# Kernel tuning notes

Hardware: AMD Instinct MI355X
Metric: run time of the kernel (lower is better)

## Reference

```python
import jax, jax.numpy as jnp
import numpy as np

H = 512       # hidden_dim == node_init_dim
N_MAX = 128   # max nodes (upper bound on ADD_NODE count)
L = 1024      # action sequence length (padded with -1)
NEG = -1e9    # mask value for invalid destination logits


def _gru(x, h, wih, whh, bih, bhh):
    # PyTorch nn.GRUCell math; gates packed as [r, z, n] along dim 0.
    gi = wih @ x + bih
    gh = whh @ h + bhh
    d = h.shape[0]
    r = jax.nn.sigmoid(gi[:d] + gh[:d])
    z = jax.nn.sigmoid(gi[d:2 * d] + gh[d:2 * d])
    n = jnp.tanh(gi[2 * d:] + r * gh[2 * d:])
    return (1.0 - z) * n + z * h


def _make_actions(rng):
    # Synthesize a grammatically valid DGMG teacher-forcing trace:
    # ADD_NODE=0, ADD_EDGE=1, CHOOSE_DEST=2, STOP_EDGE=3, STOP_NODE=4, pad=-1
    acts, ags = [], []
    cur = -1
    while len(acts) < L - 8 and cur < N_MAX - 1:
        acts.append(0); ags.append(0)
        cur += 1
        if cur > 0:
            for _ in range(int(rng.integers(1, 4))):
                if len(acts) >= L - 4:
                    break
                acts.append(1); ags.append(0)
                acts.append(2); ags.append(int(rng.integers(0, cur)))
            acts.append(3); ags.append(0)
    acts.append(4); ags.append(0)
    pad = L - len(acts)
    acts += [-1] * pad
    ags += [0] * pad
    return np.array(acts, np.int64), np.array(ags, np.int64)


def setup_inputs() -> dict:
    rng = np.random.default_rng(0)
    acts, ags = _make_actions(rng)
    key = jax.random.key(0)
    ks = jax.random.split(key, 12)
    s = 0.02
    p = lambda k, shape: jax.random.normal(k, shape, jnp.float32) * s
    return {
        "actions": jnp.asarray(acts),
        "args_seq": jnp.asarray(ags),
        "node_init": p(ks[0], (H,)),
        "w_nip": p(ks[1], (H, H)), "b_nip": jnp.zeros((H,), jnp.float32),
        "w_e1": p(ks[2], (H, 2 * H)), "b_e1": jnp.zeros((H,), jnp.float32),
        "w_e2": p(ks[3], (2, H)), "b_e2": jnp.zeros((2,), jnp.float32),
        "w_q": p(ks[4], (H, 2 * H)), "b_q": jnp.zeros((H,), jnp.float32),
        "w_k": p(ks[5], (H, H)), "b_k": jnp.zeros((H,), jnp.float32),
        "wih_n": p(ks[6], (3 * H, H)), "whh_n": p(ks[7], (3 * H, H)),
        "bih_n": jnp.zeros((3 * H,), jnp.float32), "bhh_n": jnp.zeros((3 * H,), jnp.float32),
        "wih_g": p(ks[8], (3 * H, H)), "whh_g": p(ks[9], (3 * H, H)),
        "bih_g": jnp.zeros((3 * H,), jnp.float32), "bhh_g": jnp.zeros((3 * H,), jnp.float32),
        "graph0": jnp.zeros((H,), jnp.float32),
    }


def reference(actions, args_seq, node_init, w_nip, b_nip, w_e1, b_e1, w_e2, b_e2,
              w_q, b_q, w_k, b_k, wih_n, whh_n, bih_n, bhh_n,
              wih_g, whh_g, bih_g, bhh_g, graph0):
    h0 = w_nip @ node_init + b_nip  # same fresh-node embedding for every ADD_NODE
    idx_range = jnp.arange(N_MAX)

    def edge_logits(g, curv):
        h = jax.nn.relu(w_e1 @ jnp.concatenate([g, curv]) + b_e1)
        return w_e2 @ h + b_e2  # (2,)

    def add_node(carry, arg):
        g, ne, cur, nll = carry
        cur2 = cur + 1
        ne2 = ne.at[cur2].set(h0)
        g2 = _gru(h0, g, wih_g, whh_g, bih_g, bhh_g)
        return (g2, ne2, cur2, nll)

    def add_edge(carry, arg):
        g, ne, cur, nll = carry
        nll2 = nll - jax.nn.log_softmax(edge_logits(g, ne[cur]))[0]
        return (g, ne, cur, nll2)

    def choose_dest(carry, arg):
        g, ne, cur, nll = carry
        curv = ne[cur]
        q = w_q @ jnp.concatenate([g, curv]) + b_q           # (H,)
        k = ne @ w_k.T + b_k                                  # (N_MAX, H)
        logits = jnp.where(idx_range < cur, k @ q, NEG)       # mask nodes >= cur
        nll2 = nll - jax.nn.log_softmax(logits)[arg]
        chosen = ne[arg]
        new_cur = _gru(chosen, curv, wih_n, whh_n, bih_n, bhh_n)
        ne2 = ne.at[cur].set(new_cur)
        g2 = _gru(new_cur, g, wih_g, whh_g, bih_g, bhh_g)
        return (g2, ne2, cur, nll2)

    def stop_edge(carry, arg):
        g, ne, cur, nll = carry
        nll2 = nll - jax.nn.log_softmax(edge_logits(g, ne[cur]))[1]
        return (g, ne, cur, nll2)

    def noop(carry, arg):
        return carry

    branches = [add_node, add_edge, choose_dest, stop_edge, noop]

    def step(carry, inp):
        a, arg = inp
        idx = jnp.where((a < 0) | (a >= 4), 4, a).astype(jnp.int32)
        return jax.lax.switch(idx, branches, carry, arg), None

    init = (graph0, jnp.zeros((N_MAX, H), graph0.dtype),
            jnp.int32(-1), jnp.zeros((), graph0.dtype))
    (g, ne, cur, nll), _ = jax.lax.scan(
        step, init, (actions.astype(jnp.int32), args_seq.astype(jnp.int32)))
    return nll
```

## Files before the change

### kernel.cpp

```cpp
#include <hip/hip_runtime.h>
#include <math.h>

#define NBLK 64
#define NTHR 576
#define LSEQ 1024

typedef unsigned int u32;
typedef unsigned short u16;
typedef unsigned long long u64;

__device__ __forceinline__ float bf2f(u16 u){ union{u32 i;float f;}v; v.i=(u32)u<<16; return v.f; }
__device__ __forceinline__ u16 f2bf(float f){ union{float f;u32 i;}v; v.f=f; u32 x=v.i;
  return (u16)((x + 0x7fffu + ((x>>16)&1u)) >> 16); }
__device__ __forceinline__ float u2f(u32 u){ union{u32 i;float f;}v; v.i=u; return v.f; }
__device__ __forceinline__ u32  f2u(float f){ union{float f;u32 i;}v; v.f=f; return v.i; }
__device__ __forceinline__ float sigm(float x){ return 1.f/(1.f+__expf(-x)); }

__device__ __forceinline__ u64 gld64(const u64* p){ return __hip_atomic_load(const_cast<u64*>(p), __ATOMIC_RELAXED, __HIP_MEMORY_SCOPE_AGENT); }
__device__ __forceinline__ void gst64(u64* p, u64 v){ __hip_atomic_store(p, v, __ATOMIC_RELAXED, __HIP_MEMORY_SCOPE_AGENT); }
__device__ __forceinline__ u64 pollt(const u64* p, u32 tag){
  u64 v; int n = 0;
  do { v = gld64(p); } while ((u32)(v>>32) != tag && ++n < (1<<20));
  return v;
}

__device__ __forceinline__ float wred(float a){
  a += __int_as_float(__builtin_amdgcn_update_dpp(0, __float_as_int(a), 0x111, 0xf, 0xf, true));
  a += __int_as_float(__builtin_amdgcn_update_dpp(0, __float_as_int(a), 0x112, 0xf, 0xf, true));
  a += __int_as_float(__builtin_amdgcn_update_dpp(0, __float_as_int(a), 0x114, 0xf, 0xf, true));
  a += __int_as_float(__builtin_amdgcn_update_dpp(0, __float_as_int(a), 0x118, 0xf, 0xf, true));
  a += __int_as_float(__builtin_amdgcn_update_dpp(0, __float_as_int(a), 0x142, 0xa, 0xf, true));
  a += __int_as_float(__builtin_amdgcn_update_dpp(0, __float_as_int(a), 0x143, 0xc, 0xf, true));
  return __int_as_float(__builtin_amdgcn_readlane(__float_as_int(a), 63));
}
__device__ __forceinline__ float wredsh(float a){
  #pragma unroll
  for (int off = 32; off; off >>= 1) a += __shfl_xor(a, off);
  return a;
}
__device__ __forceinline__ float wredmaxsh(float a){
  #pragma unroll
  for (int off = 32; off; off >>= 1) a = fmaxf(a, __shfl_xor(a, off));
  return a;
}

__device__ __forceinline__ float dot8p(uint4 w, float4 a, float4 b2){
  float s;
  s  = u2f(w.x<<16)*a.x  + u2f(w.x&0xffff0000u)*a.y;
  s += u2f(w.y<<16)*a.z  + u2f(w.y&0xffff0000u)*a.w;
  s += u2f(w.z<<16)*b2.x + u2f(w.z&0xffff0000u)*b2.y;
  s += u2f(w.w<<16)*b2.z + u2f(w.w&0xffff0000u)*b2.w;
  return s;
}
__device__ __forceinline__ float dot4f(float4 w, float4 x){
  return w.x*x.x + w.y*x.y + w.z*x.z + w.w*x.w;
}
__device__ __forceinline__ uint4 pk8(float4 a, float4 b2){
  uint4 r;
  r.x = (u32)f2bf(a.x)  | ((u32)f2bf(a.y)<<16);
  r.y = (u32)f2bf(a.z)  | ((u32)f2bf(a.w)<<16);
  r.z = (u32)f2bf(b2.x) | ((u32)f2bf(b2.y)<<16);
  r.w = (u32)f2bf(b2.z) | ((u32)f2bf(b2.w)<<16);
  return r;
}

#define SMEM_BYTES 150048

#define RUN_JOBS() do { \
  if (wv == 8){ \
    if (dBV && b == dBo1){ \
      u64 v_ = pollt(XS + dBSlot*64 + lane, dBTag); \
      float x0 = sA0 + bf2f((u16)(v_ & 0xffff)); \
      float x1 = sA1 + bf2f((u16)((v_>>16) & 0xffff)); \
      x0 = (lane < dBcur) ? x0 : -__builtin_inff(); \
      x1 = (lane + 64 < dBcur) ? x1 : -__builtin_inff(); \
      float m_ = wredmaxsh(fmaxf(x0, x1)); \
      float s_ = wredsh(__expf(x0 - m_) + __expf(x1 - m_)); \
      float la_ = (dBarg < 64) ? __shfl(x0, dBarg) : __shfl(x1, dBarg - 64); \
      if (lane == 0) nllw += (m_ + logf(s_)) - la_; \
    } \
    if (dAV && (b == dAo1 || b == dAo2)){ \
      const u64* P_ = XP + ((size_t)(dASlot*64 + lane))*64 + ((b == dAo2) ? 32 : 0); \
      float h0_ = 0.f, h1_ = 0.f; \
      for (int c_ = 0; c_ < 2; ++c_){ \
        u64 vv_[16]; int bad_; int nn_ = 0; \
        do { bad_ = 0; \
          _Pragma("unroll") for (int j_ = 0; j_ < 16; ++j_) vv_[j_] = gld64(P_ + c_*16 + j_); \
          _Pragma("unroll") for (int j_ = 0; j_ < 16; ++j_) bad_ |= ((u32)(vv_[j_]>>32) != dATag); \
        } while (bad_ && ++nn_ < (1<<20)); \
        _Pragma("unroll") for (int j_ = 0; j_ < 16; ++j_){ \
          h0_ += bf2f((u16)(vv_[j_] & 0xffff)); h1_ += bf2f((u16)((vv_[j_]>>16) & 0xffff)); } \
      } \
      if (b == dAo2) gst64(XS + dASlot*64 + lane, ((u64)dATag<<32) | (u32)f2bf(h0_) | ((u32)f2bf(h1_)<<16)); \
      else { sA0 = h0_; sA1 = h1_; } \
    } \
    if (aeV && b == aeOwn){ \
      u64 v_ = pollt(XE + aeSlot*64 + lane, aeTag); \
      float p0_ = wredsh(bf2f((u16)(v_ & 0xffff))); \
      float p1_ = wredsh(bf2f((u16)((v_>>16) & 0xffff))); \
      if (lane == 0){ \
        float l0_ = p0_ + be2_0, l1_ = p1_ + be2_1; \
        float m_ = fmaxf(l0_, l1_); \
        nllw += m_ + logf(__expf(l0_-m_) + __expf(l1_-m_)) - (aeSel ? l1_ : l0_); \
      } \
    } \
  } \
} while(0)

#define SHIFT_JOBS() do { \
  dBV = dAV; dBSlot = dASlot; dBo1 = dAo1; dBTag = dATag; dBcur = dAcur; dBarg = dAarg; \
  dAV = 0; aeV = 0; \
} while(0)

__global__ void __launch_bounds__(NTHR, 1)
dgmg_kernel(const int* __restrict__ actions, const int* __restrict__ argseq,
            const float* __restrict__ node_init, const float* __restrict__ w_nip, const float* __restrict__ b_nip,
            const float* __restrict__ w_e1, const float* __restrict__ b_e1,
            const float* __restrict__ w_e2, const float* __restrict__ b_e2,
            const float* __restrict__ w_q, const float* __restrict__ b_q,
            const float* __restrict__ w_k,
            const float* __restrict__ wih_n, const float* __restrict__ whh_n,
            const float* __restrict__ bih_n, const float* __restrict__ bhh_n,
            const float* __restrict__ wih_g, const float* __restrict__ whh_g,
            const float* __restrict__ bih_g, const float* __restrict__ bhh_g,
            const float* __restrict__ graph0,
            float* __restrict__ out, unsigned char* __restrict__ ws)
{
  extern __shared__ unsigned char smem[];
  u16* s_wihg = (u16*)smem;
  u16* s_whhg = s_wihg + 24*512;
  u16* s_wihn = s_whhg + 24*512;
  u16* s_whhn = s_wihn + 24*512;
  u16* s_we1  = s_whhn + 24*512;
  u16* s_wq   = s_we1 + 8*1024;
  float* s_g    = (float*)(s_wq + 8*1024);
  float* s_nc   = s_g + 512;
  float* s_curv = s_nc + 512;
  float* s_h0   = s_curv + 512;
  float* s_kloc = s_h0 + 512;
  float* s_bihg = s_kloc + 1024;
  float* s_bhhg = s_bihg + 24;
  float* s_bihn = s_bhhg + 24;
  float* s_bhhn = s_bihn + 24;
  float* s_be1  = s_bhhn + 24;
  float* s_bq   = s_be1 + 8;
  float* s_q8   = s_bq + 8;
  float* s_red  = s_q8 + 8;
  u16*   s_gin  = (u16*)(s_red + 16);

  const int b = blockIdx.x, tid = threadIdx.x;
  const int wv = tid >> 6, lane = tid & 63;
  const int d = b*8 + ((wv < 8) ? wv : 0);

  u64* Xng = (u64*)ws;
  u64* Xh  = Xng + 2048;
  u64* XE  = Xh + 512;
  u64* XP  = XE + 256;
  u64* XS  = XP + 16384;
  u64* XN  = XS + 256;

  if (tid < 24){
    int ld = tid/3, gt = tid%3;
    int row = gt*512 + b*8 + ld;
    s_bihg[tid] = bih_g[row]; s_bhhg[tid] = bhh_g[row];
    s_bihn[tid] = bih_n[row]; s_bhhn[tid] = bhh_n[row];
  }
  if (tid < 8){ s_be1[tid] = b_e1[b*8+tid]; s_bq[tid] = b_q[b*8+tid]; }

  for (int r = wv; r < 24; r += 9){
    int ld = r/3, gt = r%3;
    long grow = (long)(gt*512 + b*8 + ld) * 512;
    float4 a0, a1;
    a0 = *(const float4*)&wih_g[grow + lane*8]; a1 = *(const float4*)&wih_g[grow + lane*8 + 4];
    *(uint4*)&s_wihg[r*512 + lane*8] = pk8(a0, a1);
    a0 = *(const float4*)&whh_g[grow + lane*8]; a1 = *(const float4*)&whh_g[grow + lane*8 + 4];
    *(uint4*)&s_whhg[r*512 + lane*8] = pk8(a0, a1);
    a0 = *(const float4*)&wih_n[grow + lane*8]; a1 = *(const float4*)&wih_n[grow + lane*8 + 4];
    *(uint4*)&s_wihn[r*512 + lane*8] = pk8(a0, a1);
    a0 = *(const float4*)&whh_n[grow + lane*8]; a1 = *(const float4*)&whh_n[grow + lane*8 + 4];
    *(uint4*)&s_whhn[r*512 + lane*8] = pk8(a0, a1);
  }
  if (wv < 8){
    long grow = (long)(b*8 + wv) * 1024;
    #pragma unroll
    for (int h = 0; h < 2; ++h){
      float4 a0 = *(const float4*)&w_e1[grow + h*512 + lane*8];
      float4 a1 = *(const float4*)&w_e1[grow + h*512 + lane*8 + 4];
      *(uint4*)&s_we1[wv*1024 + h*512 + lane*8] = pk8(a0, a1);
      float4 q0 = *(const float4*)&w_q[grow + h*512 + lane*8];
      float4 q1 = *(const float4*)&w_q[grow + h*512 + lane*8 + 4];
      *(uint4*)&s_wq[wv*1024 + h*512 + lane*8] = pk8(q0, q1);
    }
  }
  float we2_0 = w_e2[d], we2_1 = w_e2[512+d];
  float be2_0 = b_e2[0], be2_1 = b_e2[1];
  float nllw = 0.f, sA0 = 0.f, sA1 = 0.f;

  int aeV=0, aeSlot=0, aeSel=0, aeOwn=0; u32 aeTag=0;
  int dAV=0, dASlot=0, dAo1=0, dAo2=0, dAcur=0, dAarg=0; u32 dATag=0;
  int dBV=0, dBSlot=0, dBo1=0, dBcur=0, dBarg=0; u32 dBTag=0;
  int ecnt=0, dcnt=0;

  if (tid < 512) s_g[tid] = node_init[tid];
  __syncthreads();
  float cbg_r=0,cbg_z=0,bg_ni=0,bg_nh=0, bh_gr=0,bh_gz=0;
  float bn_r=0,bn_z=0,bn_nh=0, fb_r=0,fb_z=0,fb_n=0, be1w=0,bqw=0;
  if (wv < 8){
    cbg_r = s_bihg[wv*3+0]+s_bhhg[wv*3+0];
    cbg_z = s_bihg[wv*3+1]+s_bhhg[wv*3+1];
    bg_ni = s_bihg[wv*3+2]; bg_nh = s_bhhg[wv*3+2];
    bh_gr = s_bhhg[wv*3+0]; bh_gz = s_bhhg[wv*3+1];
    bn_r = s_bhhn[wv*3+0]; bn_z = s_bhhn[wv*3+1]; bn_nh = s_bhhn[wv*3+2];
    fb_r = s_bihn[wv*3+0]; fb_z = s_bihn[wv*3+1]; fb_n = s_bihn[wv*3+2];
    be1w = s_be1[wv]; bqw = s_bq[wv];
    const float* wr = w_nip + (long)d*512;
    float4 wa = *(const float4*)&wr[lane*8], wb2 = *(const float4*)&wr[lane*8+4];
    float4 xa = *(float4*)&s_g[lane*8], xb = *(float4*)&s_g[lane*8+4];
    float h0d = wred(dot4f(wa,xa)+dot4f(wb2,xb)) + b_nip[d];
    if (lane == 0) gst64(&Xh[d], (1ull<<32) | f2u(h0d));
  }
  u32 ph = 2;

  float gi0r=0,gi0z=0,gi0n=0, ghn0r=0,ghn0z=0,ghn0n=0;
  int cur = -1, have_se = 0;
  bool first_an = true;

  for (int t = 0; t < LSEQ; ++t){
    int a = actions[t];
    if (a == 1) continue;
    if (a == 3){ have_se = 1; continue; }
    if (a < 0 || a >= 4) continue;

    int t1 = (t+1 < LSEQ) ? actions[t+1] : -1;
    int nxt = (t1 == 1);
    int i2 = (t+2 < LSEQ) ? t+2 : LSEQ-1;
    int chn = nxt ? argseq[i2] : 0;

    if (a == 0){
      int eslot = ecnt & 3;
      u32 tg = ph-1; int par = tg & 1;
      if (first_an){
        if (tid < 512){ u64 v = pollt(&Xh[tid], 1u); s_h0[tid] = u2f((u32)v); s_g[tid] = graph0[tid]; }
      } else {
        if (tid < 512){ u64 v = pollt(&Xng[(par*512+tid)*2+1], tg); s_g[tid] = u2f((u32)v); }
      }
      __syncthreads();
      RUN_JOBS();
      if (wv < 8){
        float4 xg_a = *(float4*)&s_g[lane*8], xg_b = *(float4*)&s_g[lane*8+4];
        float4 xc_a = *(float4*)&s_curv[lane*8], xc_b = *(float4*)&s_curv[lane*8+4];
        const u32* Whg = (const u32*)s_whhg;
        if (first_an){
          float4 xh_a = *(float4*)&s_h0[lane*8], xh_b = *(float4*)&s_h0[lane*8+4];
          const u32* Wig = (const u32*)s_wihg; const u32* Wn = (const u32*)s_whhn;
          gi0r = wred(dot8p(*(const uint4*)&Wig[(wv*3+0)*256+lane*4], xh_a,xh_b)) + s_bihg[wv*3+0];
          gi0z = wred(dot8p(*(const uint4*)&Wig[(wv*3+1)*256+lane*4], xh_a,xh_b)) + s_bihg[wv*3+1];
          gi0n = wred(dot8p(*(const uint4*)&Wig[(wv*3+2)*256+lane*4], xh_a,xh_b)) + s_bihg[wv*3+2];
          ghn0r = wred(dot8p(*(const uint4*)&Wn[(wv*3+0)*256+lane*4], xh_a,xh_b)) + bn_r;
          ghn0z = wred(dot8p(*(const uint4*)&Wn[(wv*3+1)*256+lane*4], xh_a,xh_b)) + bn_z;
          ghn0n = wred(dot8p(*(const uint4*)&Wn[(wv*3+2)*256+lane*4], xh_a,xh_b)) + bn_nh;
        }
        {
          float ghr = wred(dot8p(*(const uint4*)&Whg[(wv*3+0)*256+lane*4], xg_a,xg_b)) + bh_gr;
          float ghz = wred(dot8p(*(const uint4*)&Whg[(wv*3+1)*256+lane*4], xg_a,xg_b)) + bh_gz;
          float ghn = wred(dot8p(*(const uint4*)&Whg[(wv*3+2)*256+lane*4], xg_a,xg_b)) + bg_nh;
          float r_ = sigm(gi0r + ghr), z_ = sigm(gi0z + ghz);
          float n_ = tanhf(gi0n + r_*ghn);
          if (lane == 0) gst64(&Xng[((ph&1)*512+d)*2+1], ((u64)ph<<32) | f2u((1.f-z_)*n_ + z_*s_g[d]));
        }
        if (nxt){
          float gr = bf2f(s_gin[chn*24+wv*3+0]), gz = bf2f(s_gin[chn*24+wv*3+1]), gn = bf2f(s_gin[chn*24+wv*3+2]);
          float r2 = sigm(gr + ghn0r), z2 = sigm(gz + ghn0z);
          float n2 = tanhf(gn + r2*ghn0n);
          if (lane == 0) gst64(&Xng[((ph&1)*512+d)*2], ((u64)ph<<32) | f2u((1.f-z2)*n2 + z2*s_h0[d]));
        }
        if (cur >= 0){
          const u32* Win = (const u32*)s_wihn;
          float fr = wred(dot8p(*(const uint4*)&Win[(wv*3+0)*256+lane*4], xc_a,xc_b)) + fb_r;
          float fz = wred(dot8p(*(const uint4*)&Win[(wv*3+1)*256+lane*4], xc_a,xc_b)) + fb_z;
          float fn = wred(dot8p(*(const uint4*)&Win[(wv*3+2)*256+lane*4], xc_a,xc_b)) + fb_n;
          const float* wkr = w_k + (long)d*512;
          float4 ka = *(const float4*)&wkr[lane*8], kb2 = *(const float4*)&wkr[lane*8+4];
          float kv = wred(dot4f(ka,xc_a)+dot4f(kb2,xc_b));
          if (lane == 0){
            s_gin[cur*24+wv*3+0] = f2bf(fr); s_gin[cur*24+wv*3+1] = f2bf(fz); s_gin[cur*24+wv*3+2] = f2bf(fn);
            s_kloc[wv*128 + cur] = kv;
          }
        }
        if (have_se){
          const u32* Re = (const u32*)s_we1 + wv*512;
          float pe = dot8p(*(const uint4*)&Re[lane*4], xg_a,xg_b) + dot8p(*(const uint4*)&Re[256+lane*4], xc_a,xc_b);
          float hv = fmaxf(wred(pe) + be1w, 0.f);
          if (lane == 0){ s_red[wv*2] = hv*we2_0; s_red[wv*2+1] = hv*we2_1; }
        }
      }
      __syncthreads();
      if (have_se && tid == 0){
        float p0 = 0.f, p1 = 0.f;
        #pragma unroll
        for (int i = 0; i < 8; ++i){ p0 += s_red[i*2]; p1 += s_red[i*2+1]; }
        gst64(&XE[eslot*64 + b], ((u64)ph<<32) | (u32)f2bf(p0) | ((u32)f2bf(p1)<<16));
      }
      if (tid < 512) s_curv[tid] = s_h0[tid];
      SHIFT_JOBS();
      if (have_se){ aeV=1; aeSlot=eslot; aeSel=1; aeOwn=ecnt&63; aeTag=ph; ecnt++; }
      have_se = 0; first_an = false;
      cur += 1; ph += 1;
    }
    else {
      int arg = argseq[t];
      int eslot = ecnt & 3, dslot = dcnt & 3;
      u32 tg = ph-1; int par = tg & 1;
      if (tid < 512){
        u64 v0, v1; int n = 0;
        const u64* p = &Xng[(par*512 + tid)*2];
        do { v0 = gld64(p); v1 = gld64(p+1); }
        while ((((u32)(v0>>32) != tg) || ((u32)(v1>>32) != tg)) && ++n < (1<<20));
        s_nc[tid] = u2f((u32)v0); s_g[tid] = u2f((u32)v1);
      }
      __syncthreads();
      RUN_JOBS();
      if (wv < 8){
        float4 xn_a = *(float4*)&s_nc[lane*8], xn_b = *(float4*)&s_nc[lane*8+4];
        float4 xg_a = *(float4*)&s_g[lane*8],  xg_b = *(float4*)&s_g[lane*8+4];
        float4 xc_a = *(float4*)&s_curv[lane*8], xc_b = *(float4*)&s_curv[lane*8+4];
        const u32* Wn = (const u32*)s_whhn; const u32* Wig = (const u32*)s_wihg; const u32* Whg = (const u32*)s_whhg;
        if (nxt){
          float ghr = wred(dot8p(*(const uint4*)&Wn[(wv*3+0)*256+lane*4], xn_a,xn_b)) + bn_r;
          float ghz = wred(dot8p(*(const uint4*)&Wn[(wv*3+1)*256+lane*4], xn_a,xn_b)) + bn_z;
          float ghn = wred(dot8p(*(const uint4*)&Wn[(wv*3+2)*256+lane*4], xn_a,xn_b)) + bn_nh;
          float gr = bf2f(s_gin[chn*24+wv*3+0]), gz = bf2f(s_gin[chn*24+wv*3+1]), gn = bf2f(s_gin[chn*24+wv*3+2]);
          float r_ = sigm(gr+ghr), z_ = sigm(gz+ghz);
          float n_ = tanhf(gn + r_*ghn);
          if (lane == 0) gst64(&Xng[((ph&1)*512+d)*2], ((u64)ph<<32) | f2u((1.f-z_)*n_ + z_*s_nc[d]));
        }
        {
          float pr = dot8p(*(const uint4*)&Wig[(wv*3+0)*256+lane*4], xn_a,xn_b)
                   + dot8p(*(const uint4*)&Whg[(wv*3+0)*256+lane*4], xg_a,xg_b);
          float pz = dot8p(*(const uint4*)&Wig[(wv*3+1)*256+lane*4], xn_a,xn_b)
                   + dot8p(*(const uint4*)&Whg[(wv*3+1)*256+lane*4], xg_a,xg_b);
          float r_ = sigm(wred(pr) + cbg_r);
          float z_ = sigm(wred(pz) + cbg_z);
          float gin_ = wred(dot8p(*(const uint4*)&Wig[(wv*3+2)*256+lane*4], xn_a,xn_b)) + bg_ni;
          float ghn_ = wred(dot8p(*(const uint4*)&Whg[(wv*3+2)*256+lane*4], xg_a,xg_b)) + bg_nh;
          float n_ = tanhf(gin_ + r_*ghn_);
          if (lane == 0) gst64(&Xng[((ph&1)*512+d)*2+1], ((u64)ph<<32) | f2u((1.f-z_)*n_ + z_*s_g[d]));
        }
        {
          const u32* Rq = (const u32*)s_wq + wv*512;
          float pq = dot8p(*(const uint4*)&Rq[lane*4], xg_a,xg_b) + dot8p(*(const uint4*)&Rq[256+lane*4], xc_a,xc_b);
          float qd = wred(pq) + bqw;
          const u32* Re = (const u32*)s_we1 + wv*512;
          float pe = dot8p(*(const uint4*)&Re[lane*4], xg_a,xg_b) + dot8p(*(const uint4*)&Re[256+lane*4], xc_a,xc_b);
          float hv = fmaxf(wred(pe) + be1w, 0.f);
          if (lane == 0){ s_q8[wv] = qd; s_red[wv*2] = hv*we2_0; s_red[wv*2+1] = hv*we2_1; }
        }
      }
      __syncthreads();
      if (tid < 64){
        float pl0 = 0.f, pl1 = 0.f;
        #pragma unroll
        for (int k = 0; k < 8; ++k){
          pl0 += s_kloc[k*128 + tid]      * s_q8[k];
          pl1 += s_kloc[k*128 + tid + 64] * s_q8[k];
        }
        gst64(&XP[((size_t)(dslot*64 + tid))*64 + b], ((u64)ph<<32) | (u32)f2bf(pl0) | ((u32)f2bf(pl1)<<16));
      }
      if (tid == 64){
        float p0 = 0.f, p1 = 0.f;
        #pragma unroll
        for (int i = 0; i < 8; ++i){ p0 += s_red[i*2]; p1 += s_red[i*2+1]; }
        gst64(&XE[eslot*64 + b], ((u64)ph<<32) | (u32)f2bf(p0) | ((u32)f2bf(p1)<<16));
      }
      if (tid < 512) s_curv[tid] = s_nc[tid];
      SHIFT_JOBS();
      aeV=1; aeSlot=eslot; aeSel=0; aeOwn=ecnt&63; aeTag=ph; ecnt++;
      dAV=1; dASlot=dslot; dAo1=(2*dcnt)&63; dAo2=(2*dcnt+1)&63; dAcur=cur; dAarg=arg; dATag=ph;
      dcnt++;
      ph += 1;
    }
  }

  {
    int eslot = ecnt & 3;
    u32 tg = ph-1; int par = tg & 1;
    if (tid < 512){ u64 v = pollt(&Xng[(par*512+tid)*2+1], tg); s_g[tid] = u2f((u32)v); }
    __syncthreads();
    RUN_JOBS();
    if (have_se && wv < 8){
      float4 xg_a = *(float4*)&s_g[lane*8], xg_b = *(float4*)&s_g[lane*8+4];
      float4 xc_a = *(float4*)&s_curv[lane*8], xc_b = *(float4*)&s_curv[lane*8+4];
      const u32* Re = (const u32*)s_we1 + wv*512;
      float pe = dot8p(*(const uint4*)&Re[lane*4], xg_a,xg_b) + dot8p(*(const uint4*)&Re[256+lane*4], xc_a,xc_b);
      float hv = fmaxf(wred(pe) + be1w, 0.f);
      if (lane == 0){ s_red[wv*2] = hv*we2_0; s_red[wv*2+1] = hv*we2_1; }
    }
    __syncthreads();
    if (have_se && tid == 0){
      float p0 = 0.f, p1 = 0.f;
      #pragma unroll
      for (int i = 0; i < 8; ++i){ p0 += s_red[i*2]; p1 += s_red[i*2+1]; }
      gst64(&XE[eslot*64 + b], ((u64)ph<<32) | (u32)f2bf(p0) | ((u32)f2bf(p1)<<16));
    }
    SHIFT_JOBS();
    RUN_JOBS();
    if (wv == 8){
      if (have_se && b == 0){
        u64 v = pollt(&XE[eslot*64 + lane], ph);
        float p0 = wredsh(bf2f((u16)(v & 0xffff)));
        float p1 = wredsh(bf2f((u16)((v>>16) & 0xffff)));
        if (lane == 0){
          float l0 = p0 + be2_0, l1 = p1 + be2_1;
          float m = fmaxf(l0, l1);
          nllw += m + logf(__expf(l0-m) + __expf(l1-m)) - l1;
        }
      }
      if (lane == 0) gst64(&XN[b], (0xFFFFull<<32) | f2u(nllw));
      if (b == 0){
        u64 v = pollt(&XN[lane], 0xFFFFu);
        float tot = wredsh(u2f((u32)v));
        if (lane == 0) out[0] = tot;
      }
    }
  }
}

extern "C" void kernel_launch(void* const* d_in, const int* in_sizes, int n_in,
                              void* d_out, int out_size, void* d_ws, size_t ws_size,
                              hipStream_t stream) {
  (void)in_sizes; (void)n_in; (void)out_size; (void)ws_size;
  hipMemsetAsync(d_ws, 0, 156160, stream);
  hipFuncSetAttribute((const void*)dgmg_kernel,
                      hipFuncAttributeMaxDynamicSharedMemorySize, SMEM_BYTES);
  dgmg_kernel<<<NBLK, NTHR, SMEM_BYTES, stream>>>(
      (const int*)d_in[0], (const int*)d_in[1],
      (const float*)d_in[2], (const float*)d_in[3], (const float*)d_in[4],
      (const float*)d_in[5], (const float*)d_in[6],
      (const float*)d_in[7], (const float*)d_in[8],
      (const float*)d_in[9], (const float*)d_in[10],
      (const float*)d_in[11],
      (const float*)d_in[13], (const float*)d_in[14],
      (const float*)d_in[15], (const float*)d_in[16],
      (const float*)d_in[17], (const float*)d_in[18],
      (const float*)d_in[19], (const float*)d_in[20],
      (const float*)d_in[21],
      (float*)d_out, (unsigned char*)d_ws);
}
```

Before: 1.102 ms.

## Split auxiliary softmax/NLL jobs across extra waves with deeper pipeline

Raises the block to 11 waves and gives the edge-logit NLL, the partial-sum reduction and the dest softmax their own waves (8, 9, 10), so they no longer run back to back on one wave. The dest reduction becomes a three-stage pipeline through two XS halves, and leftover jobs are drained after the loop. It also reorders the per-step GRU work so the critical graph GRU output is published first, and reuses the freshly computed input projection when the next chosen node is the current one. The cost is more threads per block, an extra block-wide sync after init, a larger workspace, and longer latency before final NLL terms are summed.

```diff
diff --git a/kernel.cpp b/kernel.cpp
--- a/kernel.cpp
+++ b/kernel.cpp
@@ -2,7 +2,7 @@
 #include <math.h>
 
 #define NBLK 64
-#define NTHR 576
+#define NTHR 704
 #define LSEQ 1024
 
 typedef unsigned int u32;
@@ -67,49 +67,52 @@
 #define SMEM_BYTES 150048
 
 #define RUN_JOBS() do { \
-  if (wv == 8){ \
-    if (dBV && b == dBo1){ \
-      u64 v_ = pollt(XS + dBSlot*64 + lane, dBTag); \
-      float x0 = sA0 + bf2f((u16)(v_ & 0xffff)); \
-      float x1 = sA1 + bf2f((u16)((v_>>16) & 0xffff)); \
-      x0 = (lane < dBcur) ? x0 : -__builtin_inff(); \
-      x1 = (lane + 64 < dBcur) ? x1 : -__builtin_inff(); \
-      float m_ = wredmaxsh(fmaxf(x0, x1)); \
-      float s_ = wredsh(__expf(x0 - m_) + __expf(x1 - m_)); \
-      float la_ = (dBarg < 64) ? __shfl(x0, dBarg) : __shfl(x1, dBarg - 64); \
-      if (lane == 0) nllw += (m_ + logf(s_)) - la_; \
-    } \
-    if (dAV && (b == dAo1 || b == dAo2)){ \
-      const u64* P_ = XP + ((size_t)(dASlot*64 + lane))*64 + ((b == dAo2) ? 32 : 0); \
-      float h0_ = 0.f, h1_ = 0.f; \
-      for (int c_ = 0; c_ < 2; ++c_){ \
-        u64 vv_[16]; int bad_; int nn_ = 0; \
-        do { bad_ = 0; \
-          _Pragma("unroll") for (int j_ = 0; j_ < 16; ++j_) vv_[j_] = gld64(P_ + c_*16 + j_); \
-          _Pragma("unroll") for (int j_ = 0; j_ < 16; ++j_) bad_ |= ((u32)(vv_[j_]>>32) != dATag); \
-        } while (bad_ && ++nn_ < (1<<20)); \
-        _Pragma("unroll") for (int j_ = 0; j_ < 16; ++j_){ \
-          h0_ += bf2f((u16)(vv_[j_] & 0xffff)); h1_ += bf2f((u16)((vv_[j_]>>16) & 0xffff)); } \
-      } \
-      if (b == dAo2) gst64(XS + dASlot*64 + lane, ((u64)dATag<<32) | (u32)f2bf(h0_) | ((u32)f2bf(h1_)<<16)); \
-      else { sA0 = h0_; sA1 = h1_; } \
-    } \
-    if (aeV && b == aeOwn){ \
-      u64 v_ = pollt(XE + aeSlot*64 + lane, aeTag); \
-      float p0_ = wredsh(bf2f((u16)(v_ & 0xffff))); \
-      float p1_ = wredsh(bf2f((u16)((v_>>16) & 0xffff))); \
-      if (lane == 0){ \
-        float l0_ = p0_ + be2_0, l1_ = p1_ + be2_1; \
-        float m_ = fmaxf(l0_, l1_); \
-        nllw += m_ + logf(__expf(l0_-m_) + __expf(l1_-m_)) - (aeSel ? l1_ : l0_); \
-      } \
+  if (wv == 8 && d2V && (b == d2o1 || b == d2o2)){ \
+    int half_ = (b == d2o2) ? 1 : 0; \
+    const u64* P_ = XP + ((size_t)(d2Slot*64 + lane))*64 + half_*32; \
+    u64 vv_[32]; int bad_; int nn_ = 0; \
+    do { bad_ = 0; \
+      _Pragma("unroll") for (int j_ = 0; j_ < 32; ++j_) vv_[j_] = gld64(P_ + j_); \
+      _Pragma("unroll") for (int j_ = 0; j_ < 32; ++j_) bad_ |= ((u32)(vv_[j_]>>32) != d2Tag); \
+    } while (bad_ && ++nn_ < (1<<20)); \
+    float h0_ = 0.f, h1_ = 0.f; \
+    _Pragma("unroll") for (int j_ = 0; j_ < 32; ++j_){ \
+      h0_ += bf2f((u16)(vv_[j_] & 0xffff)); h1_ += bf2f((u16)((vv_[j_]>>16) & 0xffff)); } \
+    gst64(&XS[half_*256 + d2Slot*64 + lane], ((u64)d2Tag<<32) | (u32)f2bf(h0_) | ((u32)f2bf(h1_)<<16)); \
+  } \
+  if (wv == 10 && d3V && b == d3o1){ \
+    const u64* pa_ = &XS[d3Slot*64 + lane]; \
+    const u64* pb_ = &XS[256 + d3Slot*64 + lane]; \
+    u64 va_, vb_; int nn_ = 0; \
+    do { va_ = gld64(pa_); vb_ = gld64(pb_); } \
+    while ((((u32)(va_>>32) != d3Tag) || ((u32)(vb_>>32) != d3Tag)) && ++nn_ < (1<<20)); \
+    float x0 = bf2f((u16)(va_ & 0xffff)) + bf2f((u16)(vb_ & 0xffff)); \
+    float x1 = bf2f((u16)((va_>>16) & 0xffff)) + bf2f((u16)((vb_>>16) & 0xffff)); \
+    x0 = (lane < d3cur)      ? x0 : -__builtin_inff(); \
+    x1 = (lane + 64 < d3cur) ? x1 : -__builtin_inff(); \
+    float m_ = wredmaxsh(fmaxf(x0, x1)); \
+    float s_ = wredsh(__expf(x0 - m_) + __expf(x1 - m_)); \
+    float la_ = (d3arg < 64) ? __shfl(x0, d3arg) : __shfl(x1, d3arg - 64); \
+    if (lane == 0) nllw += (m_ + logf(s_)) - la_; \
+  } \
+  if (wv == 9 && e2V && b == e2Own){ \
+    u64 v_ = pollt(XE + e2Slot*64 + lane, e2Tag); \
+    float p0_ = wredsh(bf2f((u16)(v_ & 0xffff))); \
+    float p1_ = wredsh(bf2f((u16)((v_>>16) & 0xffff))); \
+    if (lane == 0){ \
+      float l0_ = p0_ + be2_0, l1_ = p1_ + be2_1; \
+      float m_ = fmaxf(l0_, l1_); \
+      nllw += m_ + logf(__expf(l0_-m_) + __expf(l1_-m_)) - (e2Sel ? l1_ : l0_); \
     } \
   } \
 } while(0)
 
-#define SHIFT_JOBS() do { \
-  dBV = dAV; dBSlot = dASlot; dBo1 = dAo1; dBTag = dATag; dBcur = dAcur; dBarg = dAarg; \
-  dAV = 0; aeV = 0; \
+#define SHIFT3() do { \
+  d3V=d2V; d3Slot=d2Slot; d3o1=d2o1; d3Tag=d2Tag; d3cur=d2cur; d3arg=d2arg; \
+  d2V=d1V; d2Slot=d1Slot; d2o1=d1o1; d2o2=d1o2; d2Tag=d1Tag; d2cur=d1cur; d2arg=d1arg; \
+  d1V=0; \
+  e2V=e1V; e2Slot=e1Slot; e2Own=e1Own; e2Tag=e1Tag; e2Sel=e1Sel; \
+  e1V=0; \
 } while(0)
 
 __global__ void __launch_bounds__(NTHR, 1)
@@ -157,7 +160,7 @@
   u64* XE  = Xh + 512;
   u64* XP  = XE + 256;
   u64* XS  = XP + 16384;
-  u64* XN  = XS + 256;
+  u64* XN  = XS + 512;
 
   if (tid < 24){
     int ld = tid/3, gt = tid%3;
@@ -167,7 +170,7 @@
   }
   if (tid < 8){ s_be1[tid] = b_e1[b*8+tid]; s_bq[tid] = b_q[b*8+tid]; }
 
-  for (int r = wv; r < 24; r += 9){
+  for (int r = wv; r < 24; r += 11){
     int ld = r/3, gt = r%3;
     long grow = (long)(gt*512 + b*8 + ld) * 512;
     float4 a0, a1;
@@ -194,11 +197,13 @@
   }
   float we2_0 = w_e2[d], we2_1 = w_e2[512+d];
   float be2_0 = b_e2[0], be2_1 = b_e2[1];
-  float nllw = 0.f, sA0 = 0.f, sA1 = 0.f;
-
-  int aeV=0, aeSlot=0, aeSel=0, aeOwn=0; u32 aeTag=0;
-  int dAV=0, dASlot=0, dAo1=0, dAo2=0, dAcur=0, dAarg=0; u32 dATag=0;
-  int dBV=0, dBSlot=0, dBo1=0, dBcur=0, dBarg=0; u32 dBTag=0;
+  float nllw = 0.f;
+
+  int d1V=0,d1Slot=0,d1o1=0,d1o2=0,d1cur=0,d1arg=0; u32 d1Tag=0;
+  int d2V=0,d2Slot=0,d2o1=0,d2o2=0,d2cur=0,d2arg=0; u32 d2Tag=0;
+  int d3V=0,d3Slot=0,d3o1=0,d3cur=0,d3arg=0; u32 d3Tag=0;
+  int e1V=0,e1Slot=0,e1Own=0,e1Sel=0; u32 e1Tag=0;
+  int e2V=0,e2Slot=0,e2Own=0,e2Sel=0; u32 e2Tag=0;
   int ecnt=0, dcnt=0;
 
   if (tid < 512) s_g[tid] = node_init[tid];
@@ -219,6 +224,7 @@
     float h0d = wred(dot4f(wa,xa)+dot4f(wb2,xb)) + b_nip[d];
     if (lane == 0) gst64(&Xh[d], (1ull<<32) | f2u(h0d));
   }
+  __syncthreads();
   u32 ph = 2;
 
   float gi0r=0,gi0z=0,gi0n=0, ghn0r=0,ghn0z=0,ghn0n=0;
@@ -236,13 +242,14 @@
     int i2 = (t+2 < LSEQ) ? t+2 : LSEQ-1;
     int chn = nxt ? argseq[i2] : 0;
 
+    u32 tg = ph-1;
+
     if (a == 0){
       int eslot = ecnt & 3;
-      u32 tg = ph-1; int par = tg & 1;
       if (first_an){
         if (tid < 512){ u64 v = pollt(&Xh[tid], 1u); s_h0[tid] = u2f((u32)v); s_g[tid] = graph0[tid]; }
       } else {
-        if (tid < 512){ u64 v = pollt(&Xng[(par*512+tid)*2+1], tg); s_g[tid] = u2f((u32)v); }
+        if (tid < 512){ u64 v = pollt(&Xng[((tg&1)*512+tid)*2+1], tg); s_g[tid] = u2f((u32)v); }
       }
       __syncthreads();
       RUN_JOBS();
@@ -268,17 +275,12 @@
           float n_ = tanhf(gi0n + r_*ghn);
           if (lane == 0) gst64(&Xng[((ph&1)*512+d)*2+1], ((u64)ph<<32) | f2u((1.f-z_)*n_ + z_*s_g[d]));
         }
-        if (nxt){
-          float gr = bf2f(s_gin[chn*24+wv*3+0]), gz = bf2f(s_gin[chn*24+wv*3+1]), gn = bf2f(s_gin[chn*24+wv*3+2]);
-          float r2 = sigm(gr + ghn0r), z2 = sigm(gz + ghn0z);
-          float n2 = tanhf(gn + r2*ghn0n);
-          if (lane == 0) gst64(&Xng[((ph&1)*512+d)*2], ((u64)ph<<32) | f2u((1.f-z2)*n2 + z2*s_h0[d]));
-        }
+        float fr=0.f, fz=0.f, fn=0.f;
         if (cur >= 0){
           const u32* Win = (const u32*)s_wihn;
-          float fr = wred(dot8p(*(const uint4*)&Win[(wv*3+0)*256+lane*4], xc_a,xc_b)) + fb_r;
-          float fz = wred(dot8p(*(const uint4*)&Win[(wv*3+1)*256+lane*4], xc_a,xc_b)) + fb_z;
-          float fn = wred(dot8p(*(const uint4*)&Win[(wv*3+2)*256+lane*4], xc_a,xc_b)) + fb_n;
+          fr = wred(dot8p(*(const uint4*)&Win[(wv*3+0)*256+lane*4], xc_a,xc_b)) + fb_r;
+          fz = wred(dot8p(*(const uint4*)&Win[(wv*3+1)*256+lane*4], xc_a,xc_b)) + fb_z;
+          fn = wred(dot8p(*(const uint4*)&Win[(wv*3+2)*256+lane*4], xc_a,xc_b)) + fb_n;
           const float* wkr = w_k + (long)d*512;
           float4 ka = *(const float4*)&wkr[lane*8], kb2 = *(const float4*)&wkr[lane*8+4];
           float kv = wred(dot4f(ka,xc_a)+dot4f(kb2,xc_b));
@@ -287,6 +289,14 @@
             s_kloc[wv*128 + cur] = kv;
           }
         }
+        if (nxt){
+          float gr = (chn == cur) ? fr : bf2f(s_gin[chn*24+wv*3+0]);
+          float gz = (chn == cur) ? fz : bf2f(s_gin[chn*24+wv*3+1]);
+          float gn = (chn == cur) ? fn : bf2f(s_gin[chn*24+wv*3+2]);
+          float r2 = sigm(gr + ghn0r), z2 = sigm(gz + ghn0z);
+          float n2 = tanhf(gn + r2*ghn0n);
+          if (lane == 0) gst64(&Xng[((ph&1)*512+d)*2], ((u64)ph<<32) | f2u((1.f-z2)*n2 + z2*s_h0[d]));
+        }
         if (have_se){
           const u32* Re = (const u32*)s_we1 + wv*512;
           float pe = dot8p(*(const uint4*)&Re[lane*4], xg_a,xg_b) + dot8p(*(const uint4*)&Re[256+lane*4], xc_a,xc_b);
@@ -302,18 +312,17 @@
         gst64(&XE[eslot*64 + b], ((u64)ph<<32) | (u32)f2bf(p0) | ((u32)f2bf(p1)<<16));
       }
       if (tid < 512) s_curv[tid] = s_h0[tid];
-      SHIFT_JOBS();
-      if (have_se){ aeV=1; aeSlot=eslot; aeSel=1; aeOwn=ecnt&63; aeTag=ph; ecnt++; }
+      SHIFT3();
+      if (have_se){ e1V=1; e1Slot=eslot; e1Sel=1; e1Own=ecnt&63; e1Tag=ph; ecnt++; }
       have_se = 0; first_an = false;
       cur += 1; ph += 1;
     }
     else {
       int arg = argseq[t];
       int eslot = ecnt & 3, dslot = dcnt & 3;
-      u32 tg = ph-1; int par = tg & 1;
       if (tid < 512){
+        const u64* p = &Xng[((tg&1)*512 + tid)*2];
         u64 v0, v1; int n = 0;
-        const u64* p = &Xng[(par*512 + tid)*2];
         do { v0 = gld64(p); v1 = gld64(p+1); }
         while ((((u32)(v0>>32) != tg) || ((u32)(v1>>32) != tg)) && ++n < (1<<20));
         s_nc[tid] = u2f((u32)v0); s_g[tid] = u2f((u32)v1);
@@ -325,15 +334,6 @@
         float4 xg_a = *(float4*)&s_g[lane*8],  xg_b = *(float4*)&s_g[lane*8+4];
         float4 xc_a = *(float4*)&s_curv[lane*8], xc_b = *(float4*)&s_curv[lane*8+4];
         const u32* Wn = (const u32*)s_whhn; const u32* Wig = (const u32*)s_wihg; const u32* Whg = (const u32*)s_whhg;
-        if (nxt){
-          float ghr = wred(dot8p(*(const uint4*)&Wn[(wv*3+0)*256+lane*4], xn_a,xn_b)) + bn_r;
-          float ghz = wred(dot8p(*(const uint4*)&Wn[(wv*3+1)*256+lane*4], xn_a,xn_b)) + bn_z;
-          float ghn = wred(dot8p(*(const uint4*)&Wn[(wv*3+2)*256+lane*4], xn_a,xn_b)) + bn_nh;
-          float gr = bf2f(s_gin[chn*24+wv*3+0]), gz = bf2f(s_gin[chn*24+wv*3+1]), gn = bf2f(s_gin[chn*24+wv*3+2]);
-          float r_ = sigm(gr+ghr), z_ = sigm(gz+ghz);
-          float n_ = tanhf(gn + r_*ghn);
-          if (lane == 0) gst64(&Xng[((ph&1)*512+d)*2], ((u64)ph<<32) | f2u((1.f-z_)*n_ + z_*s_nc[d]));
-        }
         {
           float pr = dot8p(*(const uint4*)&Wig[(wv*3+0)*256+lane*4], xn_a,xn_b)
                    + dot8p(*(const uint4*)&Whg[(wv*3+0)*256+lane*4], xg_a,xg_b);
@@ -346,6 +346,15 @@
           float n_ = tanhf(gin_ + r_*ghn_);
           if (lane == 0) gst64(&Xng[((ph&1)*512+d)*2+1], ((u64)ph<<32) | f2u((1.f-z_)*n_ + z_*s_g[d]));
         }
+        if (nxt){
+          float ghr = wred(dot8p(*(const uint4*)&Wn[(wv*3+0)*256+lane*4], xn_a,xn_b)) + bn_r;
+          float ghz = wred(dot8p(*(const uint4*)&Wn[(wv*3+1)*256+lane*4], xn_a,xn_b)) + bn_z;
+          float ghn = wred(dot8p(*(const uint4*)&Wn[(wv*3+2)*256+lane*4], xn_a,xn_b)) + bn_nh;
+          float gr = bf2f(s_gin[chn*24+wv*3+0]), gz = bf2f(s_gin[chn*24+wv*3+1]), gn = bf2f(s_gin[chn*24+wv*3+2]);
+          float r_ = sigm(gr+ghr), z_ = sigm(gz+ghz);
+          float n_ = tanhf(gn + r_*ghn);
+          if (lane == 0) gst64(&Xng[((ph&1)*512+d)*2], ((u64)ph<<32) | f2u((1.f-z_)*n_ + z_*s_nc[d]));
+        }
         {
           const u32* Rq = (const u32*)s_wq + wv*512;
           float pq = dot8p(*(const uint4*)&Rq[lane*4], xg_a,xg_b) + dot8p(*(const uint4*)&Rq[256+lane*4], xc_a,xc_b);
@@ -373,18 +382,17 @@
         gst64(&XE[eslot*64 + b], ((u64)ph<<32) | (u32)f2bf(p0) | ((u32)f2bf(p1)<<16));
       }
       if (tid < 512) s_curv[tid] = s_nc[tid];
-      SHIFT_JOBS();
-      aeV=1; aeSlot=eslot; aeSel=0; aeOwn=ecnt&63; aeTag=ph; ecnt++;
-      dAV=1; dASlot=dslot; dAo1=(2*dcnt)&63; dAo2=(2*dcnt+1)&63; dAcur=cur; dAarg=arg; dATag=ph;
-      dcnt++;
+      SHIFT3();
+      e1V=1; e1Slot=eslot; e1Sel=0; e1Own=ecnt&63; e1Tag=ph; ecnt++;
+      d1V=1; d1Slot=dslot; d1o1=(2*dcnt)&63; d1o2=(2*dcnt+1)&63; d1cur=cur; d1arg=arg; d1Tag=ph; dcnt++;
       ph += 1;
     }
   }
 
   {
     int eslot = ecnt & 3;
-    u32 tg = ph-1; int par = tg & 1;
-    if (tid < 512){ u64 v = pollt(&Xng[(par*512+tid)*2+1], tg); s_g[tid] = u2f((u32)v); }
+    u32 tg = ph-1;
+    if (tid < 512){ u64 v = pollt(&Xng[((tg&1)*512+tid)*2+1], tg); s_g[tid] = u2f((u32)v); }
     __syncthreads();
     RUN_JOBS();
     if (have_se && wv < 8){
@@ -402,26 +410,24 @@
       for (int i = 0; i < 8; ++i){ p0 += s_red[i*2]; p1 += s_red[i*2+1]; }
       gst64(&XE[eslot*64 + b], ((u64)ph<<32) | (u32)f2bf(p0) | ((u32)f2bf(p1)<<16));
     }
-    SHIFT_JOBS();
+    SHIFT3();
+    if (have_se){ e1V=1; e1Slot=eslot; e1Sel=1; e1Own=ecnt&63; e1Tag=ph; ecnt++; }
+    ph += 1;
+  }
+  #pragma unroll 1
+  for (int dp = 0; dp < 3; ++dp){
+    __syncthreads();
     RUN_JOBS();
-    if (wv == 8){
-      if (have_se && b == 0){
-        u64 v = pollt(&XE[eslot*64 + lane], ph);
-        float p0 = wredsh(bf2f((u16)(v & 0xffff)));
-        float p1 = wredsh(bf2f((u16)((v>>16) & 0xffff)));
-        if (lane == 0){
-          float l0 = p0 + be2_0, l1 = p1 + be2_1;
-          float m = fmaxf(l0, l1);
-          nllw += m + logf(__expf(l0-m) + __expf(l1-m)) - l1;
-        }
-      }
-      if (lane == 0) gst64(&XN[b], (0xFFFFull<<32) | f2u(nllw));
-      if (b == 0){
-        u64 v = pollt(&XN[lane], 0xFFFFu);
-        float tot = wredsh(u2f((u32)v));
-        if (lane == 0) out[0] = tot;
-      }
-    }
+    SHIFT3();
+    ph += 1;
+  }
+  if (wv == 9  && lane == 0) gst64(&XN[b],      (0xFFFFull<<32) | f2u(nllw));
+  if (wv == 10 && lane == 0) gst64(&XN[64 + b], (0xFFFFull<<32) | f2u(nllw));
+  if (b == 0 && wv == 8){
+    u64 va = pollt(&XN[lane], 0xFFFFu);
+    u64 vb = pollt(&XN[64 + lane], 0xFFFFu);
+    float tot = wredsh(u2f((u32)va) + u2f((u32)vb));
+    if (lane == 0) out[0] = tot;
   }
 }
 
@@ -429,7 +435,7 @@
                               void* d_out, int out_size, void* d_ws, size_t ws_size,
                               hipStream_t stream) {
   (void)in_sizes; (void)n_in; (void)out_size; (void)ws_size;
-  hipMemsetAsync(d_ws, 0, 156160, stream);
+  hipMemsetAsync(d_ws, 0, 158720, stream);
   hipFuncSetAttribute((const void*)dgmg_kernel,
                       hipFuncAttributeMaxDynamicSharedMemorySize, SMEM_BYTES);
   dgmg_kernel<<<NBLK, NTHR, SMEM_BYTES, stream>>>(
```

Measured after the change: 1.220 ms. +10.7%, slower.
